# Kernel tuning notes

Measured on AMD Instinct MI355X. Metric: run time of the kernel, lower is better.

## Reference

```python
import jax, jax.numpy as jnp
import numpy as np

SCORE_THRESH = 0.05
NMS_THRESH = 0.5
MAX_DET = 100
N_BOXES = 8192


def setup_inputs() -> dict:
    key = jax.random.key(0)
    k1, k2, k3, k4, k5 = jax.random.split(key, 5)
    N = N_BOXES
    # well-formed axis-aligned boxes (x1,y1,x2,y2) plus 8 keypoint coords
    xy = jax.random.uniform(k1, (N, 2)) * 1000.0
    wh = jax.random.uniform(k2, (N, 2)) * 120.0 + 4.0
    kp = jax.random.uniform(k3, (N, 8)) * 1000.0
    boxes = jnp.concatenate([xy, xy + wh, kp], axis=1)            # (N, 12)
    classification = jax.random.uniform(k4, (N, 8))               # two heads x 4 orientations
    dimensions = jax.random.uniform(k5, (N, 3)) * 4.0             # (h, w, l) for the single class
    return {"boxes": boxes, "dimensions": dimensions, "classification": classification}


def _nms_keep(b4, scores, valid):
    """Greedy NMS. Returns (order, keep) where order sorts by score desc and
    keep[i] says whether the i-th sorted box survives."""
    N = b4.shape[0]
    order = jnp.argsort(-jnp.where(valid, scores, -jnp.inf))
    bs = b4[order]                                                 # (N, 4) sorted boxes
    vs = valid[order]
    x1, y1, x2, y2 = bs[:, 0], bs[:, 1], bs[:, 2], bs[:, 3]
    area = (x2 - x1) * (y2 - y1)
    iw = jnp.clip(jnp.minimum(x2[:, None], x2[None, :]) - jnp.maximum(x1[:, None], x1[None, :]), 0.0)
    ih = jnp.clip(jnp.minimum(y2[:, None], y2[None, :]) - jnp.maximum(y1[:, None], y1[None, :]), 0.0)
    inter = iw * ih                                                # (N, N)
    iou = inter / jnp.maximum(area[:, None] + area[None, :] - inter, 1e-8)
    idx = jnp.arange(N)

    def body(keep, xs):
        row, v, i = xs
        suppressed = jnp.any(keep & (row > NMS_THRESH) & (idx < i))
        keep = keep.at[i].set(v & jnp.logical_not(suppressed))
        return keep, None

    keep, _ = jax.lax.scan(body, jnp.zeros((N,), dtype=bool), (iou, vs, idx))
    return order, keep


def reference(boxes, dimensions, classification):
    # max over the two classification heads -> per-orientation score (N, 4)
    cls2 = jnp.maximum(classification[:, :4], classification[:, 4:])
    orient = jnp.argmax(cls2, axis=1)                              # best orientation per box
    score = jnp.max(cls2, axis=1)                                  # best-orientation score
    valid = score > SCORE_THRESH

    order, keep = _nms_keep(boxes[:, :4], score, valid)
    sorted_score = jnp.where(keep, score[order], -jnp.inf)
    top_scores, top_pos = jax.lax.top_k(sorted_score, MAX_DET)     # top-k among kept
    sel = order[top_pos]                                           # original box indices
    ok = jnp.isfinite(top_scores)                                  # real detections vs -1 padding

    out_boxes = jnp.where(ok[:, None], boxes[sel], -1.0)           # (MAX_DET, 12)
    out_dims = jnp.where(ok[:, None], dimensions[sel, :3], -1.0)   # (MAX_DET, 3)
    out_scores = jnp.where(ok, score[sel], -1.0)                   # (MAX_DET,)
    out_labels = jnp.where(ok, 0, -1).astype(jnp.int32)            # single class -> label 0
    out_orient = jnp.where(ok, orient[sel], -1).astype(jnp.int32)
    return out_boxes, out_dims, out_scores, out_labels, out_orient
```

## Files before the change

kernel.cpp:

```cpp
#include <hip/hip_runtime.h>

#define NBOX 8192
#define MAXDET 100
#define SCORE_T 0.05f
#define NMS_T 0.5f
#define CAP 1024
#define KTGT 128
#define BT2 256

typedef unsigned long long u64;

#define WS_KEYS 1024
#define WS_KIDX 33792
#define WS_FB0  41984

__device__ __forceinline__ float iou_fn(float x1, float y1, float x2, float y2, float area,
                                        float bx1, float by1, float bx2, float by2, float barea) {
    float iw = fminf(x2, bx2) - fmaxf(x1, bx1);
    float ih = fminf(y2, by2) - fmaxf(y1, by1);
    iw = fmaxf(iw, 0.0f);
    ih = fmaxf(ih, 0.0f);
    float inter = iw * ih;
    return inter / fmaxf(area + barea - inter, 1e-8f);
}

__device__ __forceinline__ void bins_of(unsigned k, int& b1, int& b2) {
    float s = __uint_as_float(k & 0x7FFFFFFFu);
    b1 = (int)(s * 256.0f); if (b1 > 255) b1 = 255;
    b2 = (int)(s * 65536.0f) & 255;
}

__global__ __launch_bounds__(128) void score_push_kernel(
    const float* __restrict__ boxes, const float* __restrict__ cls,
    unsigned* __restrict__ keys, unsigned* __restrict__ cnt,
    u64* __restrict__ kidx, float4* __restrict__ fb0) {
    const int i = blockIdx.x * 128 + threadIdx.x;
    const float4 c0 = *reinterpret_cast<const float4*>(cls + i * 8);
    const float4 c1 = *reinterpret_cast<const float4*>(cls + i * 8 + 4);
    float s = fmaxf(fmaxf(fmaxf(c0.x, c1.x), fmaxf(c0.y, c1.y)),
                    fmaxf(fmaxf(c0.z, c1.z), fmaxf(c0.w, c1.w)));
    unsigned u = __float_as_uint(s);
    unsigned key = (u >> 31) ? ~u : (u | 0x80000000u);
    key = (s > SCORE_T) ? key : 0u;
    keys[i] = key;
    int b1 = (int)(s * 256.0f); if (b1 > 255) b1 = 255;
    if (key && b1 == 255) {
        unsigned pos = atomicAdd(cnt, 1u);
        if (pos < CAP) {
            kidx[pos] = (((u64)key) << 13) | (unsigned)(NBOX - 1 - i);
            fb0[pos] = *reinterpret_cast<const float4*>(boxes + i * 12);
        }
    }
}

__global__ __launch_bounds__(BT2) void select_nms_kernel(
    const float* __restrict__ boxes, const float* __restrict__ dims,
    const float* __restrict__ cls, const unsigned* __restrict__ keysG,
    const unsigned* __restrict__ cntG, const u64* __restrict__ kidxG,
    const float4* __restrict__ fb0G, float* __restrict__ out) {
    __shared__ unsigned s_key[NBOX];
    __shared__ unsigned s_hist[256];
    __shared__ u64 s_sel[CAP];
    __shared__ u64 s_srt[CAP];
    __shared__ unsigned short s_srtpos[CAP];
    __shared__ float4 s_cb[CAP];
    __shared__ float s_kx1[MAXDET], s_ky1[MAXDET], s_kx2[MAXDET], s_ky2[MAXDET];
    __shared__ float s_karea[MAXDET], s_kscore[MAXDET];
    __shared__ int s_ksel[MAXDET];
    __shared__ float s_bx1[128], s_by1[128], s_bx2[128], s_by2[128], s_bar[128];
    __shared__ int s_kc, s_cnt, s_B1, s_B2, s_state, s_refKrem;
    __shared__ u64 s_alive0;

    const int tid = threadIdx.x;
    const int lane = tid & 63;
    const int wid = tid >> 6;

    auto nms_groups = [&](int scN) {
        for (int base = 0; base < scN && s_kc < MAXDET; base += 128) {
            const int kc0 = s_kc;
            float x1 = 0.f, y1 = 0.f, x2 = 0.f, y2 = 0.f, area = 0.f, sscore = 0.f;
            int sidx = 0; bool have = false;
            if (wid < 2) {
                int p = base + wid * 64 + lane;
                have = p < scN;
                u64 v = have ? s_srt[p] : 0ull;
                int cp = have ? (int)s_srtpos[p] : 0;
                sidx = NBOX - 1 - (int)(v & 8191ull);
                sscore = __uint_as_float(((unsigned)(v >> 13)) & 0x7FFFFFFFu);
                float4 b = s_cb[cp];
                if (have) { x1 = b.x; y1 = b.y; x2 = b.z; y2 = b.w; area = (x2 - x1) * (y2 - y1); }
                int sl = wid * 64 + lane;
                s_bx1[sl] = x1; s_by1[sl] = y1; s_bx2[sl] = x2; s_by2[sl] = y2; s_bar[sl] = area;
            }
            __syncthreads();
            if (wid == 0) {
                bool cand = have;
                for (int k = 0; k < kc0; ++k) {
                    float iou = iou_fn(x1, y1, x2, y2, area,
                                       s_kx1[k], s_ky1[k], s_kx2[k], s_ky2[k], s_karea[k]);
                    cand = cand && !(iou > NMS_T);
                }
                u64 m = 0ull;
#pragma unroll 4
                for (int j = 0; j < 64; ++j) {
                    float iou = iou_fn(x1, y1, x2, y2, area,
                                       s_bx1[j], s_by1[j], s_bx2[j], s_by2[j], s_bar[j]);
                    if ((iou > NMS_T) && (j < lane)) m |= (1ull << j);
                }
                u64 alive = __ballot(cand);
                u64 conf = __ballot((m & alive) != 0ull) & alive;
                while (conf) {
                    int i = (int)__builtin_ctzll(conf);
                    bool deadI = (lane == i) && ((m & alive) != 0ull);
                    u64 d = __ballot(deadI);
                    alive &= ~d; conf &= ~(d | (1ull << i));
                }
                int rank = (int)__popcll(alive & ((1ull << lane) - 1ull));
                int slot = kc0 + rank;
                if (((alive >> lane) & 1ull) && slot < MAXDET) {
                    s_kx1[slot] = x1; s_ky1[slot] = y1; s_kx2[slot] = x2; s_ky2[slot] = y2;
                    s_karea[slot] = area; s_kscore[slot] = sscore; s_ksel[slot] = sidx;
                }
                if (lane == 0) s_alive0 = alive;
            }
            u64 m_low = 0ull, m_high = 0ull;
            bool cand1 = have;
            if (wid == 1) {
                for (int k = 0; k < kc0; ++k) {
                    float iou = iou_fn(x1, y1, x2, y2, area,
                                       s_kx1[k], s_ky1[k], s_kx2[k], s_ky2[k], s_karea[k]);
                    cand1 = cand1 && !(iou > NMS_T);
                }
#pragma unroll 4
                for (int j = 0; j < 64; ++j) {
                    float iou = iou_fn(x1, y1, x2, y2, area,
                                       s_bx1[j], s_by1[j], s_bx2[j], s_by2[j], s_bar[j]);
                    if (iou > NMS_T) m_low |= (1ull << j);
                }
#pragma unroll 4
                for (int j = 0; j < 64; ++j) {
                    float iou = iou_fn(x1, y1, x2, y2, area,
                                       s_bx1[64 + j], s_by1[64 + j], s_bx2[64 + j], s_by2[64 + j], s_bar[64 + j]);
                    if ((iou > NMS_T) && (j < lane)) m_high |= (1ull << j);
                }
            }
            __syncthreads();
            if (wid == 1) {
                u64 alive0 = s_alive0;
                int popc0 = (int)__popcll(alive0);
                bool cand = cand1 && ((m_low & alive0) == 0ull);
                u64 alive = __ballot(cand);
                u64 conf = __ballot((m_high & alive) != 0ull) & alive;
                while (conf) {
                    int i = (int)__builtin_ctzll(conf);
                    bool deadI = (lane == i) && ((m_high & alive) != 0ull);
                    u64 d = __ballot(deadI);
                    alive &= ~d; conf &= ~(d | (1ull << i));
                }
                int rank = (int)__popcll(alive & ((1ull << lane) - 1ull));
                int slot = kc0 + popc0 + rank;
                if (((alive >> lane) & 1ull) && slot < MAXDET) {
                    s_kx1[slot] = x1; s_ky1[slot] = y1; s_kx2[slot] = x2; s_ky2[slot] = y2;
                    s_karea[slot] = area; s_kscore[slot] = sscore; s_ksel[slot] = sidx;
                }
                if (lane == 0) {
                    int nk = kc0 + popc0 + (int)__popcll(alive);
                    s_kc = nk > MAXDET ? MAXDET : nk;
                }
            }
            __syncthreads();
        }
    };

    const unsigned cnt = *cntG;
    if (tid == 0) { s_kc = 0; s_cnt = 0; }
    int U1 = (cnt > CAP) ? 256 : 255;
    int U2 = 0;

    if (cnt > 0u && cnt <= CAP) {
        const int sc = (int)cnt;
        for (int t = tid; t < sc; t += BT2) { s_sel[t] = kidxG[t]; s_cb[t] = fb0G[t]; }
        __syncthreads();
        for (int t = tid; t < sc; t += BT2) {
            u64 mine = s_sel[t];
            int rank = 0;
            for (int j = 0; j < sc; ++j) rank += (s_sel[j] > mine) ? 1 : 0;
            s_srt[rank] = mine; s_srtpos[rank] = (unsigned short)t;
        }
        __syncthreads();
        nms_groups(sc);
    }
    __syncthreads();

    if (s_kc < MAXDET) {
        {
            const uint4* kp = reinterpret_cast<const uint4*>(keysG);
            uint4* sk = reinterpret_cast<uint4*>(s_key);
#pragma unroll
            for (int j = 0; j < NBOX / 4 / BT2; ++j) sk[tid + j * BT2] = kp[tid + j * BT2];
        }
        s_hist[tid] = 0u;
        if (tid == 0) s_cnt = 0;
        __syncthreads();
        for (int j = 0; j < NBOX / BT2; ++j) {
            unsigned k = s_key[tid + j * BT2];
            if (k) {
                int b1, b2; bins_of(k, b1, b2);
                if (b1 < U1 || (b1 == U1 && b2 < U2)) atomicAdd(&s_hist[b1], 1u);
            }
        }
        while (true) {
            __syncthreads();
            if (wid == 0) {
                unsigned c0 = s_hist[lane * 4 + 0], c1s = s_hist[lane * 4 + 1];
                unsigned c2 = s_hist[lane * 4 + 2], c3 = s_hist[lane * 4 + 3];
                unsigned t3 = c3, t2 = c2 + t3, t1 = c1s + t2, t0 = c0 + t1;
                unsigned acc = t0;
#pragma unroll
                for (int d = 1; d < 64; d <<= 1) {
                    unsigned o = __shfl_down(acc, d);
                    if (lane + d < 64) acc += o;
                }
                unsigned excl = acc - t0;
                unsigned totalRem = __shfl(acc, 0);
                if (lane == 0) s_state = (totalRem == 0u) ? 2 : 0;
                if (totalRem != 0u) {
                    unsigned Kt = totalRem < (unsigned)KTGT ? totalRem : (unsigned)KTGT;
                    unsigned incq[4] = { excl + t0, excl + t1, excl + t2, excl + t3 };
                    unsigned abvq[4] = { excl + t1, excl + t2, excl + t3, excl };
#pragma unroll
                    for (int q = 0; q < 4; ++q) {
                        if (incq[q] >= Kt && abvq[q] < Kt) {
                            s_B1 = lane * 4 + q; s_B2 = 0;
                            if (incq[q] > CAP) { s_state = 1; s_refKrem = (int)(Kt - abvq[q]); }
                        }
                    }
                }
            }
            __syncthreads();
            const int st = s_state;
            if (st == 2) break;
            const int B1 = s_B1;
            if (st == 1) {
                s_hist[tid] = 0u;
                __syncthreads();
                for (int j = 0; j < NBOX / BT2; ++j) {
                    unsigned k = s_key[tid + j * BT2];
                    if (k) {
                        int b1, b2; bins_of(k, b1, b2);
                        if ((b1 < U1 || (b1 == U1 && b2 < U2)) && b1 == B1)
                            atomicAdd(&s_hist[b2], 1u);
                    }
                }
                __syncthreads();
                if (wid == 0) {
                    unsigned c0 = s_hist[lane * 4 + 0], c1s = s_hist[lane * 4 + 1];
                    unsigned c2 = s_hist[lane * 4 + 2], c3 = s_hist[lane * 4 + 3];
                    unsigned t3 = c3, t2 = c2 + t3, t1 = c1s + t2, t0 = c0 + t1;
                    unsigned acc = t0;
#pragma unroll
                    for (int d = 1; d < 64; d <<= 1) {
                        unsigned o = __shfl_down(acc, d);
                        if (lane + d < 64) acc += o;
                    }
                    unsigned excl = acc - t0;
                    unsigned Krem = (unsigned)s_refKrem;
                    unsigned incq[4] = { excl + t0, excl + t1, excl + t2, excl + t3 };
                    unsigned abvq[4] = { excl + t1, excl + t2, excl + t3, excl };
#pragma unroll
                    for (int q = 0; q < 4; ++q)
                        if (incq[q] >= Krem && abvq[q] < Krem) s_B2 = lane * 4 + q;
                }
                __syncthreads();
            }
            const int B2 = s_B2;
            for (int j = 0; j < NBOX / BT2; ++j) {
                int i = tid + j * BT2;
                unsigned k = s_key[i];
                if (k) {
                    int b1, b2; bins_of(k, b1, b2);
                    bool inr = (b1 < U1) || (b1 == U1 && b2 < U2);
                    bool sel = inr && ((b1 > B1) || (b1 == B1 && b2 >= B2));
                    if (sel) {
                        int pos = atomicAdd(&s_cnt, 1);
                        if (pos < CAP)
                            s_sel[pos] = (((u64)k) << 13) | (unsigned)(NBOX - 1 - i);
                    }
                }
            }
            __syncthreads();
            const int sc2 = s_cnt < CAP ? s_cnt : CAP;
            for (int t = tid; t < sc2; t += BT2) {
                u64 mine = s_sel[t];
                int bidx = NBOX - 1 - (int)(mine & 8191ull);
                s_cb[t] = *reinterpret_cast<const float4*>(boxes + bidx * 12);
                int rank = 0;
                for (int j = 0; j < sc2; ++j) rank += (s_sel[j] > mine) ? 1 : 0;
                s_srt[rank] = mine; s_srtpos[rank] = (unsigned short)t;
            }
            __syncthreads();
            nms_groups(sc2);
            if (s_kc >= MAXDET) break;
            U1 = B1; U2 = B2;
            s_hist[tid] = 0u;
            if (tid == 0) s_cnt = 0;
            __syncthreads();
            for (int j = 0; j < NBOX / BT2; ++j) {
                unsigned k = s_key[tid + j * BT2];
                if (k) {
                    int b1, b2; bins_of(k, b1, b2);
                    if (b1 < U1 || (b1 == U1 && b2 < U2)) atomicAdd(&s_hist[b1], 1u);
                }
            }
        }
    }
    __syncthreads();

    if (tid < MAXDET) {
        const int kc = s_kc;
        float* ob = out;
        float* od = out + MAXDET * 12;
        float* os = out + MAXDET * 15;
        float* ol = out + MAXDET * 16;
        float* oo = out + MAXDET * 17;
        float4* obr = reinterpret_cast<float4*>(ob + tid * 12);
        if (tid < kc) {
            int sel = s_ksel[tid];
            const float4* br = reinterpret_cast<const float4*>(boxes + sel * 12);
            obr[0] = br[0]; obr[1] = br[1]; obr[2] = br[2];
            od[tid * 3 + 0] = dims[sel * 3 + 0];
            od[tid * 3 + 1] = dims[sel * 3 + 1];
            od[tid * 3 + 2] = dims[sel * 3 + 2];
            os[tid] = s_kscore[tid];
            ol[tid] = 0.0f;
            const float4 c0 = *reinterpret_cast<const float4*>(cls + sel * 8);
            const float4 c1 = *reinterpret_cast<const float4*>(cls + sel * 8 + 4);
            float m0 = fmaxf(c0.x, c1.x);
            float m1 = fmaxf(c0.y, c1.y);
            float m2 = fmaxf(c0.z, c1.z);
            float m3 = fmaxf(c0.w, c1.w);
            int o = 0; float best = m0;
            if (m1 > best) { best = m1; o = 1; }
            if (m2 > best) { best = m2; o = 2; }
            if (m3 > best) { best = m3; o = 3; }
            oo[tid] = (float)o;
        } else {
            const float4 neg1 = make_float4(-1.f, -1.f, -1.f, -1.f);
            obr[0] = neg1; obr[1] = neg1; obr[2] = neg1;
            od[tid * 3 + 0] = -1.0f; od[tid * 3 + 1] = -1.0f; od[tid * 3 + 2] = -1.0f;
            os[tid] = -1.0f; ol[tid] = -1.0f; oo[tid] = -1.0f;
        }
    }
}

extern "C" void kernel_launch(void* const* d_in, const int* in_sizes, int n_in,
                              void* d_out, int out_size, void* d_ws, size_t ws_size,
                              hipStream_t stream) {
    const float* boxes = (const float*)d_in[0];
    const float* dims  = (const float*)d_in[1];
    const float* cls   = (const float*)d_in[2];
    float* out = (float*)d_out;
    unsigned char* ws = (unsigned char*)d_ws;
    unsigned* cnt  = (unsigned*)(ws);
    unsigned* keys = (unsigned*)(ws + WS_KEYS);
    u64* kidx      = (u64*)(ws + WS_KIDX);
    float4* fb0    = (float4*)(ws + WS_FB0);
    (void)in_sizes; (void)n_in; (void)out_size; (void)ws_size;
    hipMemsetAsync(cnt, 0, sizeof(unsigned), stream);
    score_push_kernel<<<NBOX / 128, 128, 0, stream>>>(boxes, cls, keys, cnt, kidx, fb0);
    select_nms_kernel<<<1, BT2, 0, stream>>>(boxes, dims, cls, keys, cnt, kidx, fb0, out);
}
```

Baseline: 31.69 us.

## Fuse score kernel into single 1024-thread block and drop memset

Merges the score/key computation and top-bin candidate gathering into the single NMS block, which now runs with 1024 threads. This removes the memset, a second kernel launch and the global workspace round trip for keys, candidates and boxes. It also parallelises the rank sort one candidate per thread with an unrolled compare loop, and uses readlane broadcasts and float4 shared layouts in the IoU mask loops. The cost is that the whole 8192-box score pass now runs on a single workgroup rather than across many blocks.

```diff
diff --git a/kernel.cpp b/kernel.cpp
--- a/kernel.cpp
+++ b/kernel.cpp
@@ -1,18 +1,19 @@
 #include <hip/hip_runtime.h>
 
 #define NBOX 8192
+#define BT 1024
 #define MAXDET 100
 #define SCORE_T 0.05f
 #define NMS_T 0.5f
 #define CAP 1024
 #define KTGT 128
-#define BT2 256
+#define TOPBIN_T 0.99609375f
 
 typedef unsigned long long u64;
 
-#define WS_KEYS 1024
-#define WS_KIDX 33792
-#define WS_FB0  41984
+__device__ __forceinline__ float rl_f(float v, int j) {
+    return __int_as_float(__builtin_amdgcn_readlane(__float_as_int(v), j));
+}
 
 __device__ __forceinline__ float iou_fn(float x1, float y1, float x2, float y2, float area,
                                         float bx1, float by1, float bx2, float by2, float barea) {
@@ -30,50 +31,49 @@
     b2 = (int)(s * 65536.0f) & 255;
 }
 
-__global__ __launch_bounds__(128) void score_push_kernel(
-    const float* __restrict__ boxes, const float* __restrict__ cls,
-    unsigned* __restrict__ keys, unsigned* __restrict__ cnt,
-    u64* __restrict__ kidx, float4* __restrict__ fb0) {
-    const int i = blockIdx.x * 128 + threadIdx.x;
-    const float4 c0 = *reinterpret_cast<const float4*>(cls + i * 8);
-    const float4 c1 = *reinterpret_cast<const float4*>(cls + i * 8 + 4);
-    float s = fmaxf(fmaxf(fmaxf(c0.x, c1.x), fmaxf(c0.y, c1.y)),
-                    fmaxf(fmaxf(c0.z, c1.z), fmaxf(c0.w, c1.w)));
-    unsigned u = __float_as_uint(s);
-    unsigned key = (u >> 31) ? ~u : (u | 0x80000000u);
-    key = (s > SCORE_T) ? key : 0u;
-    keys[i] = key;
-    int b1 = (int)(s * 256.0f); if (b1 > 255) b1 = 255;
-    if (key && b1 == 255) {
-        unsigned pos = atomicAdd(cnt, 1u);
-        if (pos < CAP) {
-            kidx[pos] = (((u64)key) << 13) | (unsigned)(NBOX - 1 - i);
-            fb0[pos] = *reinterpret_cast<const float4*>(boxes + i * 12);
-        }
-    }
-}
-
-__global__ __launch_bounds__(BT2) void select_nms_kernel(
+__global__ __launch_bounds__(BT) void filterdet_kernel(
     const float* __restrict__ boxes, const float* __restrict__ dims,
-    const float* __restrict__ cls, const unsigned* __restrict__ keysG,
-    const unsigned* __restrict__ cntG, const u64* __restrict__ kidxG,
-    const float4* __restrict__ fb0G, float* __restrict__ out) {
+    const float* __restrict__ cls, float* __restrict__ out) {
     __shared__ unsigned s_key[NBOX];
     __shared__ unsigned s_hist[256];
     __shared__ u64 s_sel[CAP];
     __shared__ u64 s_srt[CAP];
     __shared__ unsigned short s_srtpos[CAP];
     __shared__ float4 s_cb[CAP];
-    __shared__ float s_kx1[MAXDET], s_ky1[MAXDET], s_kx2[MAXDET], s_ky2[MAXDET];
+    __shared__ float4 s_bb[128];
+    __shared__ float s_bar[128];
+    __shared__ float4 s_kb[MAXDET];
     __shared__ float s_karea[MAXDET], s_kscore[MAXDET];
     __shared__ int s_ksel[MAXDET];
-    __shared__ float s_bx1[128], s_by1[128], s_bx2[128], s_by2[128], s_bar[128];
     __shared__ int s_kc, s_cnt, s_B1, s_B2, s_state, s_refKrem;
     __shared__ u64 s_alive0;
 
     const int tid = threadIdx.x;
     const int lane = tid & 63;
     const int wid = tid >> 6;
+
+    auto rank_scatter = [&](int sc, bool loadBox) {
+        if (tid < sc) {
+            u64 mine = s_sel[tid];
+            float4 pb = make_float4(0.f, 0.f, 0.f, 0.f);
+            if (loadBox) {
+                int bidx = NBOX - 1 - (int)(mine & 8191ull);
+                pb = *reinterpret_cast<const float4*>(boxes + bidx * 12);
+            }
+            int rank = 0;
+            int j = 0;
+            for (; j + 8 <= sc; j += 8) {
+                u64 a0 = s_sel[j + 0], a1 = s_sel[j + 1], a2 = s_sel[j + 2], a3 = s_sel[j + 3];
+                u64 a4 = s_sel[j + 4], a5 = s_sel[j + 5], a6 = s_sel[j + 6], a7 = s_sel[j + 7];
+                rank += (int)(a0 > mine) + (int)(a1 > mine) + (int)(a2 > mine) + (int)(a3 > mine)
+                      + (int)(a4 > mine) + (int)(a5 > mine) + (int)(a6 > mine) + (int)(a7 > mine);
+            }
+            for (; j < sc; ++j) rank += (s_sel[j] > mine) ? 1 : 0;
+            s_srt[rank] = mine;
+            s_srtpos[rank] = (unsigned short)tid;
+            if (loadBox) s_cb[tid] = pb;
+        }
+    };
 
     auto nms_groups = [&](int scN) {
         for (int base = 0; base < scN && s_kc < MAXDET; base += 128) {
@@ -90,21 +90,21 @@
                 float4 b = s_cb[cp];
                 if (have) { x1 = b.x; y1 = b.y; x2 = b.z; y2 = b.w; area = (x2 - x1) * (y2 - y1); }
                 int sl = wid * 64 + lane;
-                s_bx1[sl] = x1; s_by1[sl] = y1; s_bx2[sl] = x2; s_by2[sl] = y2; s_bar[sl] = area;
+                s_bb[sl] = make_float4(x1, y1, x2, y2); s_bar[sl] = area;
             }
             __syncthreads();
             if (wid == 0) {
                 bool cand = have;
                 for (int k = 0; k < kc0; ++k) {
-                    float iou = iou_fn(x1, y1, x2, y2, area,
-                                       s_kx1[k], s_ky1[k], s_kx2[k], s_ky2[k], s_karea[k]);
+                    float4 kb = s_kb[k];
+                    float iou = iou_fn(x1, y1, x2, y2, area, kb.x, kb.y, kb.z, kb.w, s_karea[k]);
                     cand = cand && !(iou > NMS_T);
                 }
                 u64 m = 0ull;
-#pragma unroll 4
+#pragma unroll 8
                 for (int j = 0; j < 64; ++j) {
                     float iou = iou_fn(x1, y1, x2, y2, area,
-                                       s_bx1[j], s_by1[j], s_bx2[j], s_by2[j], s_bar[j]);
+                                       rl_f(x1, j), rl_f(y1, j), rl_f(x2, j), rl_f(y2, j), rl_f(area, j));
                     if ((iou > NMS_T) && (j < lane)) m |= (1ull << j);
                 }
                 u64 alive = __ballot(cand);
@@ -118,7 +118,7 @@
                 int rank = (int)__popcll(alive & ((1ull << lane) - 1ull));
                 int slot = kc0 + rank;
                 if (((alive >> lane) & 1ull) && slot < MAXDET) {
-                    s_kx1[slot] = x1; s_ky1[slot] = y1; s_kx2[slot] = x2; s_ky2[slot] = y2;
+                    s_kb[slot] = make_float4(x1, y1, x2, y2);
                     s_karea[slot] = area; s_kscore[slot] = sscore; s_ksel[slot] = sidx;
                 }
                 if (lane == 0) s_alive0 = alive;
@@ -127,20 +127,20 @@
             bool cand1 = have;
             if (wid == 1) {
                 for (int k = 0; k < kc0; ++k) {
-                    float iou = iou_fn(x1, y1, x2, y2, area,
-                                       s_kx1[k], s_ky1[k], s_kx2[k], s_ky2[k], s_karea[k]);
+                    float4 kb = s_kb[k];
+                    float iou = iou_fn(x1, y1, x2, y2, area, kb.x, kb.y, kb.z, kb.w, s_karea[k]);
                     cand1 = cand1 && !(iou > NMS_T);
                 }
-#pragma unroll 4
+#pragma unroll 8
+                for (int j = 0; j < 64; ++j) {
+                    float4 bb = s_bb[j];
+                    float iou = iou_fn(x1, y1, x2, y2, area, bb.x, bb.y, bb.z, bb.w, s_bar[j]);
+                    if (iou > NMS_T) m_low |= (1ull << j);
+                }
+#pragma unroll 8
                 for (int j = 0; j < 64; ++j) {
                     float iou = iou_fn(x1, y1, x2, y2, area,
-                                       s_bx1[j], s_by1[j], s_bx2[j], s_by2[j], s_bar[j]);
-                    if (iou > NMS_T) m_low |= (1ull << j);
-                }
-#pragma unroll 4
-                for (int j = 0; j < 64; ++j) {
-                    float iou = iou_fn(x1, y1, x2, y2, area,
-                                       s_bx1[64 + j], s_by1[64 + j], s_bx2[64 + j], s_by2[64 + j], s_bar[64 + j]);
+                                       rl_f(x1, j), rl_f(y1, j), rl_f(x2, j), rl_f(y2, j), rl_f(area, j));
                     if ((iou > NMS_T) && (j < lane)) m_high |= (1ull << j);
                 }
             }
@@ -160,7 +160,7 @@
                 int rank = (int)__popcll(alive & ((1ull << lane) - 1ull));
                 int slot = kc0 + popc0 + rank;
                 if (((alive >> lane) & 1ull) && slot < MAXDET) {
-                    s_kx1[slot] = x1; s_ky1[slot] = y1; s_kx2[slot] = x2; s_ky2[slot] = y2;
+                    s_kb[slot] = make_float4(x1, y1, x2, y2);
                     s_karea[slot] = area; s_kscore[slot] = sscore; s_ksel[slot] = sidx;
                 }
                 if (lane == 0) {
@@ -172,38 +172,56 @@
         }
     };
 
-    const unsigned cnt = *cntG;
+    unsigned keyr[8];
+#pragma unroll
+    for (int j = 0; j < 8; ++j) {
+        int i = tid + j * BT;
+        const float4 c0 = *reinterpret_cast<const float4*>(cls + i * 8);
+        const float4 c1 = *reinterpret_cast<const float4*>(cls + i * 8 + 4);
+        float s = fmaxf(fmaxf(fmaxf(c0.x, c1.x), fmaxf(c0.y, c1.y)),
+                        fmaxf(fmaxf(c0.z, c1.z), fmaxf(c0.w, c1.w)));
+        unsigned u = __float_as_uint(s);
+        unsigned key = (u >> 31) ? ~u : (u | 0x80000000u);
+        key = (s > SCORE_T) ? key : 0u;
+        keyr[j] = key;
+        s_key[i] = key;
+    }
     if (tid == 0) { s_kc = 0; s_cnt = 0; }
-    int U1 = (cnt > CAP) ? 256 : 255;
+    __syncthreads();
+#pragma unroll
+    for (int j = 0; j < 8; ++j) {
+        unsigned k = keyr[j];
+        if (k) {
+            float s = __uint_as_float(k & 0x7FFFFFFFu);
+            if (s >= TOPBIN_T) {
+                int pos = atomicAdd(&s_cnt, 1);
+                if (pos < CAP) {
+                    int i = tid + j * BT;
+                    s_sel[pos] = (((u64)k) << 13) | (unsigned)(NBOX - 1 - i);
+                    s_cb[pos] = *reinterpret_cast<const float4*>(boxes + i * 12);
+                }
+            }
+        }
+    }
+    __syncthreads();
+    const int cnt0 = s_cnt;
+    const bool ovf = cnt0 > CAP;
+
+    if (!ovf && cnt0 > 0) {
+        rank_scatter(cnt0, false);
+        __syncthreads();
+        nms_groups(cnt0);
+    }
+
+    int U1 = ovf ? 256 : 255;
     int U2 = 0;
 
-    if (cnt > 0u && cnt <= CAP) {
-        const int sc = (int)cnt;
-        for (int t = tid; t < sc; t += BT2) { s_sel[t] = kidxG[t]; s_cb[t] = fb0G[t]; }
-        __syncthreads();
-        for (int t = tid; t < sc; t += BT2) {
-            u64 mine = s_sel[t];
-            int rank = 0;
-            for (int j = 0; j < sc; ++j) rank += (s_sel[j] > mine) ? 1 : 0;
-            s_srt[rank] = mine; s_srtpos[rank] = (unsigned short)t;
-        }
-        __syncthreads();
-        nms_groups(sc);
-    }
-    __syncthreads();
-
     if (s_kc < MAXDET) {
-        {
-            const uint4* kp = reinterpret_cast<const uint4*>(keysG);
-            uint4* sk = reinterpret_cast<uint4*>(s_key);
-#pragma unroll
-            for (int j = 0; j < NBOX / 4 / BT2; ++j) sk[tid + j * BT2] = kp[tid + j * BT2];
-        }
-        s_hist[tid] = 0u;
+        if (tid < 256) s_hist[tid] = 0u;
         if (tid == 0) s_cnt = 0;
         __syncthreads();
-        for (int j = 0; j < NBOX / BT2; ++j) {
-            unsigned k = s_key[tid + j * BT2];
+        for (int j = 0; j < NBOX / BT; ++j) {
+            unsigned k = s_key[tid + j * BT];
             if (k) {
                 int b1, b2; bins_of(k, b1, b2);
                 if (b1 < U1 || (b1 == U1 && b2 < U2)) atomicAdd(&s_hist[b1], 1u);
@@ -242,10 +260,10 @@
             if (st == 2) break;
             const int B1 = s_B1;
             if (st == 1) {
-                s_hist[tid] = 0u;
+                if (tid < 256) s_hist[tid] = 0u;
                 __syncthreads();
-                for (int j = 0; j < NBOX / BT2; ++j) {
-                    unsigned k = s_key[tid + j * BT2];
+                for (int j = 0; j < NBOX / BT; ++j) {
+                    unsigned k = s_key[tid + j * BT];
                     if (k) {
                         int b1, b2; bins_of(k, b1, b2);
                         if ((b1 < U1 || (b1 == U1 && b2 < U2)) && b1 == B1)
@@ -274,8 +292,8 @@
                 __syncthreads();
             }
             const int B2 = s_B2;
-            for (int j = 0; j < NBOX / BT2; ++j) {
-                int i = tid + j * BT2;
+            for (int j = 0; j < NBOX / BT; ++j) {
+                int i = tid + j * BT;
                 unsigned k = s_key[i];
                 if (k) {
                     int b1, b2; bins_of(k, b1, b2);
@@ -290,23 +308,16 @@
             }
             __syncthreads();
             const int sc2 = s_cnt < CAP ? s_cnt : CAP;
-            for (int t = tid; t < sc2; t += BT2) {
-                u64 mine = s_sel[t];
-                int bidx = NBOX - 1 - (int)(mine & 8191ull);
-                s_cb[t] = *reinterpret_cast<const float4*>(boxes + bidx * 12);
-                int rank = 0;
-                for (int j = 0; j < sc2; ++j) rank += (s_sel[j] > mine) ? 1 : 0;
-                s_srt[rank] = mine; s_srtpos[rank] = (unsigned short)t;
-            }
+            rank_scatter(sc2, true);
             __syncthreads();
             nms_groups(sc2);
             if (s_kc >= MAXDET) break;
             U1 = B1; U2 = B2;
-            s_hist[tid] = 0u;
+            if (tid < 256) s_hist[tid] = 0u;
             if (tid == 0) s_cnt = 0;
             __syncthreads();
-            for (int j = 0; j < NBOX / BT2; ++j) {
-                unsigned k = s_key[tid + j * BT2];
+            for (int j = 0; j < NBOX / BT; ++j) {
+                unsigned k = s_key[tid + j * BT];
                 if (k) {
                     int b1, b2; bins_of(k, b1, b2);
                     if (b1 < U1 || (b1 == U1 && b2 < U2)) atomicAdd(&s_hist[b1], 1u);
@@ -360,13 +371,6 @@
     const float* dims  = (const float*)d_in[1];
     const float* cls   = (const float*)d_in[2];
     float* out = (float*)d_out;
-    unsigned char* ws = (unsigned char*)d_ws;
-    unsigned* cnt  = (unsigned*)(ws);
-    unsigned* keys = (unsigned*)(ws + WS_KEYS);
-    u64* kidx      = (u64*)(ws + WS_KIDX);
-    float4* fb0    = (float4*)(ws + WS_FB0);
-    (void)in_sizes; (void)n_in; (void)out_size; (void)ws_size;
-    hipMemsetAsync(cnt, 0, sizeof(unsigned), stream);
-    score_push_kernel<<<NBOX / 128, 128, 0, stream>>>(boxes, cls, keys, cnt, kidx, fb0);
-    select_nms_kernel<<<1, BT2, 0, stream>>>(boxes, dims, cls, keys, cnt, kidx, fb0, out);
-}
+    (void)in_sizes; (void)n_in; (void)out_size; (void)d_ws; (void)ws_size;
+    filterdet_kernel<<<1, BT, 0, stream>>>(boxes, dims, cls, out);
+}
```

After: 27.01 us. 14.8% less time.
